# Optimization experiments

Measured on AMD Instinct MI355X. Metric: run time of the kernel, lower is better.

## Reference

```python
import jax, jax.numpy as jnp
import numpy as np

DEGREE = 30
ORDER = 3                      # cubic-ish B-spline order used by the module
N_COEF = DEGREE + ORDER - 1    # 32 coefficients, matches compute_starting_values
SPLINE_RANGE = (-15.0, 15.0)
SPAN_FACTOR = 0.1
LOG_2PI = float(np.log(2.0 * np.pi))


def _knots():
    """Uniform knot grid expanded by span_factor, as in gtm's bspline helpers."""
    rmin, rmax = SPLINE_RANGE
    pad = (rmax - rmin) * SPAN_FACTOR
    lo, hi = rmin - pad, rmax + pad
    dist = (hi - lo) / (N_COEF - ORDER)
    i = jnp.arange(N_COEF + ORDER + 1, dtype=jnp.float32)
    return lo + (i - ORDER) * dist, lo, dist


def _deboor(x, span, knots, coefs, p):
    """Vectorized deBoor: x [N], span [N] with knots[span] <= x < knots[span+1]."""
    d = [coefs[span - p + j] for j in range(p + 1)]  # gather p+1 local coefs
    for r in range(1, p + 1):
        for j in range(p, r - 1, -1):
            kl = knots[span + j - p]
            kr = knots[span + 1 + j - r]
            alpha = (x - kl) / (kr - kl)
            d[j] = (1.0 - alpha) * d[j - 1] + alpha * d[j]
    return d[p]


def _bspline_value_and_deriv(params, y):
    # monotonic restriction: c0 = params[0], c_k = c0 + sum softplus(params[1:k+1])
    coefs = jnp.concatenate(
        [params[:1], params[0] + jnp.cumsum(jax.nn.softplus(params[1:]))]
    )
    knots, lo, dist = _knots()
    # 'reluler' span restriction: clamp inputs into the spline range
    x = jnp.clip(y, SPLINE_RANGE[0], SPLINE_RANGE[1])
    span = jnp.clip(
        jnp.floor((x - lo) / dist).astype(jnp.int32) + ORDER, ORDER, N_COEF - 1
    )
    val = _deboor(x, span, knots, coefs, ORDER)
    # derivative spline: degree p-1, coefs p*(c[i+1]-c[i])/(t[i+p+1]-t[i+1])
    dcoefs = ORDER * (coefs[1:] - coefs[:-1]) / (
        knots[ORDER + 1 : ORDER + N_COEF] - knots[1:N_COEF]
    )
    der = _deboor(x, span - 1, knots[1:-1], dcoefs, ORDER - 1)
    return val, der


def setup_inputs() -> dict:
    key = jax.random.key(0)
    k1, k2 = jax.random.split(key)
    params = jax.random.normal(k1, (N_COEF,), dtype=jnp.float32)
    y = jax.random.normal(k2, (20_000_000,), dtype=jnp.float32)
    return {"params": params, "y": y}


def reference(params, y):
    z_tilde, der_1 = _bspline_value_and_deriv(params, y)
    # Normal(0,1).log_prob(z) + log(der_1)
    return -0.5 * z_tilde * z_tilde - 0.5 * LOG_2PI + jnp.log(der_1)
```

## Files before the change

### kernel.cpp

```cpp
#include <hip/hip_runtime.h>
#include <math.h>

#define SP_INV_DIST (29.0f / 36.0f)
#define SP_U_OFFS   (17.5f)
#define NEG_HALF_LOG_2PI (-0.91893853320467274f)

typedef float f32x4 __attribute__((ext_vector_type(4)));

__device__ __forceinline__ float eval_one(float xin, const float4* __restrict__ tab) {
    float x = fminf(fmaxf(xin, -15.0f), 15.0f);
    float u = fmaf(x, SP_INV_DIST, SP_U_OFFS);
    int   s = (int)u;
    float f = u - (float)s;
    float4 a = tab[s];
    float val = fmaf(fmaf(fmaf(a.w, f, a.z), f, a.y), f, a.x);
    float der = fmaf(f, fmaf(f, 3.0f * a.w, 2.0f * a.z), a.y) * SP_INV_DIST;
    return fmaf(-0.5f * val, val, NEG_HALF_LOG_2PI) + __logf(der);
}

__global__ __launch_bounds__(256) void TM_73727408603569_kernel(
        const float* __restrict__ y, const float* __restrict__ params,
        float* __restrict__ out, int n4, int tail_base, int tail) {
    __shared__ float4 tab[32];
    int t = threadIdx.x;

    if (t < 64) {
        bool lane_p = (t >= 1 && t < 32);
        float p  = lane_p ? params[t] : 0.0f;
        float sp = lane_p ? ((p > 0.0f) ? (p + log1pf(expf(-p)))
                                        : log1pf(expf(p)))
                          : 0.0f;
        #pragma unroll
        for (int d = 1; d < 32; d <<= 1) {
            float o = __shfl_up(sp, d, 64);
            if (t >= d) sp += o;
        }
        float c  = params[0] + sp;
        float d0 = __shfl_up(c, 3, 64);
        float d1 = __shfl_up(c, 2, 64);
        float d2 = __shfl_up(c, 1, 64);
        float d3 = c;
        if (t < 32) {
            float4 vp = make_float4(0.f, 0.f, 0.f, 0.f);
            if (t >= 3) {
                const float SIXTH = 1.0f / 6.0f;
                vp.x = (d0 + 4.0f * d1 + d2) * SIXTH;
                vp.y = (d2 - d0) * 0.5f;
                vp.z = (d0 - 2.0f * d1 + d2) * 0.5f;
                vp.w = (d3 - d0 + 3.0f * (d1 - d2)) * SIXTH;
            }
            tab[t] = vp;
        }
    }
    __syncthreads();

    const f32x4* y4 = reinterpret_cast<const f32x4*>(y);
    f32x4*       o4 = reinterpret_cast<f32x4*>(out);

    int i0 = blockIdx.x * 1024 + t;
    int i1 = i0 + 256, i2 = i0 + 512, i3 = i0 + 768;
    bool p0 = i0 < n4, p1 = i1 < n4, p2 = i2 < n4, p3 = i3 < n4;
    f32x4 v0, v1, v2, v3;
    if (p0) v0 = y4[i0];
    if (p1) v1 = y4[i1];
    if (p2) v2 = y4[i2];
    if (p3) v3 = y4[i3];

    if (p0) {
        f32x4 r;
        r.x = eval_one(v0.x, tab); r.y = eval_one(v0.y, tab);
        r.z = eval_one(v0.z, tab); r.w = eval_one(v0.w, tab);
        o4[i0] = r;
    }
    if (p1) {
        f32x4 r;
        r.x = eval_one(v1.x, tab); r.y = eval_one(v1.y, tab);
        r.z = eval_one(v1.z, tab); r.w = eval_one(v1.w, tab);
        o4[i1] = r;
    }
    if (p2) {
        f32x4 r;
        r.x = eval_one(v2.x, tab); r.y = eval_one(v2.y, tab);
        r.z = eval_one(v2.z, tab); r.w = eval_one(v2.w, tab);
        o4[i2] = r;
    }
    if (p3) {
        f32x4 r;
        r.x = eval_one(v3.x, tab); r.y = eval_one(v3.y, tab);
        r.z = eval_one(v3.z, tab); r.w = eval_one(v3.w, tab);
        o4[i3] = r;
    }

    if (blockIdx.x == 0 && t < tail) {
        int idx = tail_base + t;
        out[idx] = eval_one(y[idx], tab);
    }
}

extern "C" void kernel_launch(void* const* d_in, const int* in_sizes, int n_in,
                              void* d_out, int out_size, void* d_ws, size_t ws_size,
                              hipStream_t stream) {
    const float* params = (const float*)d_in[0];
    const float* y      = (const float*)d_in[1];
    float*       out    = (float*)d_out;
    int n    = in_sizes[1];
    int n4   = n >> 2;
    int tail = n & 3;

    int blocks = (n4 + 1023) / 1024;
    if (blocks < 1) blocks = 1;
    TM_73727408603569_kernel<<<blocks, 256, 0, stream>>>(y, params, out, n4,
                                                         n4 << 2, tail);
}
```

Baseline: 35.50 us.

## Use persistent grid-stride loop with software-prefetched loads and folded constants

The one-shot grid of 1024-element blocks becomes a grid of at most 2048 blocks. Each block walks the array with a stride, loading the next pair of float4 vectors before evaluating and storing the current pair, so loads overlap with compute. The derivative scale factor is folded into the log constant, and the clamp uses a single med3 instruction. In exchange the grid is smaller, so less parallelism hides latency and the per-block table setup runs fewer times.

```diff
diff --git a/kernel.cpp b/kernel.cpp
--- a/kernel.cpp
+++ b/kernel.cpp
@@ -3,19 +3,26 @@
 
 #define SP_INV_DIST (29.0f / 36.0f)
 #define SP_U_OFFS   (17.5f)
-#define NEG_HALF_LOG_2PI (-0.91893853320467274f)
+#define C_CONST (-1.13516164467f)
 
 typedef float f32x4 __attribute__((ext_vector_type(4)));
 
 __device__ __forceinline__ float eval_one(float xin, const float4* __restrict__ tab) {
-    float x = fminf(fmaxf(xin, -15.0f), 15.0f);
+    float x = __builtin_amdgcn_fmed3f(xin, -15.0f, 15.0f);
     float u = fmaf(x, SP_INV_DIST, SP_U_OFFS);
     int   s = (int)u;
     float f = u - (float)s;
     float4 a = tab[s];
     float val = fmaf(fmaf(fmaf(a.w, f, a.z), f, a.y), f, a.x);
-    float der = fmaf(f, fmaf(f, 3.0f * a.w, 2.0f * a.z), a.y) * SP_INV_DIST;
-    return fmaf(-0.5f * val, val, NEG_HALF_LOG_2PI) + __logf(der);
+    float der = fmaf(f, fmaf(f, 3.0f * a.w, a.z + a.z), a.y);
+    return fmaf(-0.5f * val, val, C_CONST) + __logf(der);
+}
+
+__device__ __forceinline__ f32x4 eval4(f32x4 v, const float4* __restrict__ tab) {
+    f32x4 r;
+    r.x = eval_one(v.x, tab); r.y = eval_one(v.y, tab);
+    r.z = eval_one(v.z, tab); r.w = eval_one(v.w, tab);
+    return r;
 }
 
 __global__ __launch_bounds__(256) void TM_73727408603569_kernel(
@@ -57,38 +64,28 @@
     const f32x4* y4 = reinterpret_cast<const f32x4*>(y);
     f32x4*       o4 = reinterpret_cast<f32x4*>(out);
 
-    int i0 = blockIdx.x * 1024 + t;
-    int i1 = i0 + 256, i2 = i0 + 512, i3 = i0 + 768;
-    bool p0 = i0 < n4, p1 = i1 < n4, p2 = i2 < n4, p3 = i3 < n4;
-    f32x4 v0, v1, v2, v3;
-    if (p0) v0 = y4[i0];
-    if (p1) v1 = y4[i1];
-    if (p2) v2 = y4[i2];
-    if (p3) v3 = y4[i3];
+    const int S    = gridDim.x << 9;
+    const int bb   = blockIdx.x << 9;
+    int niter = (n4 > bb) ? ((n4 - 1 - bb) / S + 1) : 0;
 
-    if (p0) {
-        f32x4 r;
-        r.x = eval_one(v0.x, tab); r.y = eval_one(v0.y, tab);
-        r.z = eval_one(v0.z, tab); r.w = eval_one(v0.w, tab);
-        o4[i0] = r;
-    }
-    if (p1) {
-        f32x4 r;
-        r.x = eval_one(v1.x, tab); r.y = eval_one(v1.y, tab);
-        r.z = eval_one(v1.z, tab); r.w = eval_one(v1.w, tab);
-        o4[i1] = r;
-    }
-    if (p2) {
-        f32x4 r;
-        r.x = eval_one(v2.x, tab); r.y = eval_one(v2.y, tab);
-        r.z = eval_one(v2.z, tab); r.w = eval_one(v2.w, tab);
-        o4[i2] = r;
-    }
-    if (p3) {
-        f32x4 r;
-        r.x = eval_one(v3.x, tab); r.y = eval_one(v3.y, tab);
-        r.z = eval_one(v3.z, tab); r.w = eval_one(v3.w, tab);
-        o4[i3] = r;
+    int  i0 = bb + t, i1 = i0 + 256;
+    bool q0 = i0 < n4, q1 = i1 < n4;
+    f32x4 c0, c1;
+    if (niter > 0) {
+        if (q0) c0 = y4[i0];
+        if (q1) c1 = y4[i1];
+        for (int k = 1; k < niter; ++k) {
+            int  j0 = i0 + S, j1 = i1 + S;
+            bool r0 = j0 < n4, r1 = j1 < n4;
+            f32x4 nx0, nx1;
+            if (r0) nx0 = y4[j0];
+            if (r1) nx1 = y4[j1];
+            if (q0) o4[i0] = eval4(c0, tab);
+            if (q1) o4[i1] = eval4(c1, tab);
+            i0 = j0; i1 = j1; q0 = r0; q1 = r1; c0 = nx0; c1 = nx1;
+        }
+        if (q0) o4[i0] = eval4(c0, tab);
+        if (q1) o4[i1] = eval4(c1, tab);
     }
 
     if (blockIdx.x == 0 && t < tail) {
@@ -107,7 +104,8 @@
     int n4   = n >> 2;
     int tail = n & 3;
 
-    int blocks = (n4 + 1023) / 1024;
+    int blocks = (n4 + 511) / 512;
+    if (blocks > 2048) blocks = 2048;
     if (blocks < 1) blocks = 1;
     TM_73727408603569_kernel<<<blocks, 256, 0, stream>>>(y, params, out, n4,
                                                          n4 << 2, tail);
```

Result: faster. 31.32 us (-11.8%).
